# Optimization experiments

Hardware: AMD Instinct MI355X
Metric: run time of the kernel (lower is better)

## Reference

```python
import jax, jax.numpy as jnp
import numpy as np

EMBED_DIM = 1024
NUM_HEADS = 16
HEAD_DIM = EMBED_DIM // NUM_HEADS


def setup_inputs() -> dict:
    key = jax.random.key(0)
    kx, kw1, kb1, kw2, kb2 = jax.random.split(key, 5)
    D = EMBED_DIM
    # torch nn.Linear default init: U(-1/sqrt(in), 1/sqrt(in)); use scaled uniform
    lim = 1.0 / np.sqrt(D)
    return {
        "x": jax.random.normal(kx, (2, 2048, D), dtype=jnp.float32),
        "w_qkv": jax.random.uniform(kw1, (D, 3 * D), jnp.float32, -lim, lim),
        "b_qkv": jax.random.uniform(kb1, (3 * D,), jnp.float32, -lim, lim),
        "w_o": jax.random.uniform(kw2, (D, D), jnp.float32, -lim, lim),
        "b_o": jax.random.uniform(kb2, (D,), jnp.float32, -lim, lim),
    }


def reference(x, w_qkv, b_qkv, w_o, b_o):
    B, S, D = x.shape
    H, hd = NUM_HEADS, HEAD_DIM
    qkv = x @ w_qkv + b_qkv                       # [B,S,3D]
    qkv = qkv.reshape(B, S, H, 3, hd)             # per-head [q|k|v] blocks of size hd
    q = qkv[:, :, :, 0].transpose(0, 2, 1, 3)     # [B,H,S,hd]
    k = qkv[:, :, :, 1].transpose(0, 2, 1, 3)
    v = qkv[:, :, :, 2].transpose(0, 2, 1, 3)
    scale = hd ** -0.5
    scores = jnp.einsum('bhqd,bhkd->bhqk', q, k) * scale
    attn = jax.nn.softmax(scores, axis=-1)
    out = jnp.einsum('bhqk,bhkd->bhqd', attn, v)  # [B,H,S,hd]
    out = out.transpose(0, 2, 1, 3).reshape(B, S, D)
    return out @ w_o + b_o
```

## Files before the change

kernel.cpp:

```cpp
#include <hip/hip_runtime.h>

typedef __attribute__((ext_vector_type(8))) _Float16 half8;
typedef __attribute__((ext_vector_type(4))) _Float16 half4;
typedef __attribute__((ext_vector_type(4))) float f32x4;
typedef __attribute__((ext_vector_type(16))) float f32x16;
typedef __attribute__((ext_vector_type(4))) int i32x4;

typedef __attribute__((address_space(1))) void* gptr_t;
typedef __attribute__((address_space(3))) void* lptr_t;
#define GLL16(g, l) __builtin_amdgcn_global_load_lds((gptr_t)(g), (lptr_t)(l), 16, 0, 0)

__device__ __forceinline__ float fast_exp2(float x) {
  float r;
  asm volatile("v_exp_f32 %0, %1" : "=v"(r) : "v"(x));
  return r;
}


__global__ void prep_kernel(const float* __restrict__ x, _Float16* __restrict__ xh,
                            const float* __restrict__ w_qkv, _Float16* __restrict__ wqkvT,
                            const float* __restrict__ w_o, _Float16* __restrict__ woT) {
  __shared__ _Float16 lds[64][72];
  const int bid = blockIdx.x;
  const int t = threadIdx.x;
  if (bid < 4096) {
    size_t i = (size_t)bid * 256 + t;
    float4 v = *reinterpret_cast<const float4*>(x + i * 4);
    half4 o = { (_Float16)v.x, (_Float16)v.y, (_Float16)v.z, (_Float16)v.w };
    *reinterpret_cast<half4*>(xh + i * 4) = o;
    return;
  }
  const float* w; _Float16* wt; int N, bx, by;
  if (bid < 4096 + 768) { int b = bid - 4096; w = w_qkv; wt = wqkvT; N = 3072; bx = b % 48; by = b / 48; }
  else                  { int b = bid - 4864; w = w_o;   wt = woT;   N = 1024; bx = b & 15; by = b >> 4; }
  const int n0 = bx * 64, k0 = by * 64;
#pragma unroll
  for (int rep = 0; rep < 4; ++rep) {
    int k = rep * 16 + (t >> 4);
    int nc = (t & 15) * 4;
    float4 v = *reinterpret_cast<const float4*>(&w[(size_t)(k0 + k) * N + n0 + nc]);
    lds[nc + 0][k] = (_Float16)v.x;
    lds[nc + 1][k] = (_Float16)v.y;
    lds[nc + 2][k] = (_Float16)v.z;
    lds[nc + 3][k] = (_Float16)v.w;
  }
  __syncthreads();
#pragma unroll
  for (int rep = 0; rep < 2; ++rep) {
    int ch = rep * 256 + t;
    int n = ch >> 3, kc = ch & 7;
    half8 o = *reinterpret_cast<const half8*>(&lds[n][kc * 8]);
    *reinterpret_cast<half8*>(&wt[(size_t)(n0 + n) * 1024 + k0 + kc * 8]) = o;
  }
}


__global__ __launch_bounds__(256, 4)
void gemm_qkv(const _Float16* __restrict__ A, const _Float16* __restrict__ Bt,
              const float* __restrict__ bias,
              _Float16* __restrict__ qh, _Float16* __restrict__ kh,
              _Float16* __restrict__ vT) {
  __shared__ __align__(16) _Float16 Ah[128 * 64];
  __shared__ __align__(16) _Float16 Bh[128 * 64];
  const int t = threadIdx.x;
  const int w = t >> 6, ln = t & 63, G = ln >> 4, c = ln & 15;
  const int lid = blockIdx.y * 24 + blockIdx.x;
  const int swz = (lid & 7) * 96 + (lid >> 3);
  const int bx = swz % 24, by = swz / 24;
  const int m0 = by * 128, n0 = bx * 128;
  const int wr = w >> 1, wc = w & 1;
  f32x4 acc[4][4] = {};
  for (int kt = 0; kt < 1024; kt += 64) {
#pragma unroll
    for (int i = 0; i < 4; ++i) {
      int ch = i * 256 + t;
      int row = ch >> 3, kc = ch & 7;
      int kk = kt + ((kc ^ (row & 7)) << 3);
      int ldsbase = (i * 256 + w * 64) * 8;
      GLL16(A + (size_t)(m0 + row) * 1024 + kk, Ah + ldsbase);
      GLL16(Bt + (size_t)(n0 + row) * 1024 + kk, Bh + ldsbase);
    }
    __syncthreads();
    half8 aF[2][4], bF[2][4];
#pragma unroll
    for (int ks = 0; ks < 2; ++ks)
#pragma unroll
      for (int i = 0; i < 4; ++i) {
        int ra = wr * 64 + i * 16 + c;
        aF[ks][i] = *reinterpret_cast<const half8*>(&Ah[ra * 64 + (((ks * 4 + G) ^ (ra & 7)) << 3)]);
        int rb = wc * 64 + i * 16 + c;
        bF[ks][i] = *reinterpret_cast<const half8*>(&Bh[rb * 64 + (((ks * 4 + G) ^ (rb & 7)) << 3)]);
      }
#pragma unroll
    for (int ks = 0; ks < 2; ++ks)
#pragma unroll
      for (int mi = 0; mi < 4; ++mi)
#pragma unroll
        for (int ni = 0; ni < 4; ++ni)
          acc[mi][ni] = __builtin_amdgcn_mfma_f32_16x16x32_f16(aF[ks][mi], bF[ks][ni], acc[mi][ni], 0, 0, 0);
    __syncthreads();
  }
  const int mbase = m0 + wr * 64, nbase = n0 + wc * 64;
  const int Gp = ((G & 1) << 1) | (G >> 1);
#pragma unroll
  for (int ni = 0; ni < 4; ++ni) {
    int n = nbase + ni * 16 + c;
    float bv = bias[n];
    int h = n / 192;
    int rem = n - h * 192;
    int tt = rem >> 6, d = rem & 63;
#pragma unroll
    for (int mi = 0; mi < 4; ++mi) {
      if (tt == 2) {
        int mb = mbase + mi * 16;
        int bb = mb >> 11, s0 = mb & 2047;
        size_t bh = (size_t)(bb * 16 + h);
        half4 o = { (_Float16)(acc[mi][ni][0] + bv), (_Float16)(acc[mi][ni][1] + bv),
                    (_Float16)(acc[mi][ni][2] + bv), (_Float16)(acc[mi][ni][3] + bv) };
        *reinterpret_cast<half4*>(&vT[(bh * 64 + d) * 2048 + s0 + 4 * Gp]) = o;
      } else {
#pragma unroll
        for (int r = 0; r < 4; ++r) {
          int m = mbase + mi * 16 + 4 * G + r;
          int bb = m >> 11, s = m & 2047;
          float val = acc[mi][ni][r] + bv;
          size_t bh = (size_t)(bb * 16 + h);
          if (tt == 0) qh[(bh * 2048 + s) * 64 + d] = (_Float16)(val * (0.125f * 1.44269504089f));
          else         kh[(bh * 2048 + s) * 64 + d] = (_Float16)val;
        }
      }
    }
  }
}


__global__ __launch_bounds__(256, 4)
void gemm_o(const _Float16* __restrict__ A, const _Float16* __restrict__ Bt,
            const float* __restrict__ bias, float* __restrict__ outf) {
  __shared__ __align__(16) _Float16 Ah[128 * 64];
  __shared__ __align__(16) _Float16 Bh[64 * 64];
  const int t = threadIdx.x;
  const int w = t >> 6, ln = t & 63, G = ln >> 4, c = ln & 15;
  const int lid = blockIdx.y * 16 + blockIdx.x;
  const int swz = (lid & 7) * 64 + (lid >> 3);
  const int bx = swz & 15, by = swz >> 4;
  const int m0 = by * 128, n0 = bx * 64;
  const int wr = w >> 1, wc = w & 1;
  f32x4 acc[4][2] = {};
  for (int kt = 0; kt < 1024; kt += 64) {
#pragma unroll
    for (int i = 0; i < 4; ++i) {
      int ch = i * 256 + t;
      int row = ch >> 3, kc = ch & 7;
      int kk = kt + ((kc ^ (row & 7)) << 3);
      GLL16(A + (size_t)(m0 + row) * 1024 + kk, Ah + (i * 256 + w * 64) * 8);
    }
#pragma unroll
    for (int i = 0; i < 2; ++i) {
      int ch = i * 256 + t;
      int row = ch >> 3, kc = ch & 7;
      int kk = kt + ((kc ^ (row & 7)) << 3);
      GLL16(Bt + (size_t)(n0 + row) * 1024 + kk, Bh + (i * 256 + w * 64) * 8);
    }
    __syncthreads();
    half8 aF[2][4], bF[2][2];
#pragma unroll
    for (int ks = 0; ks < 2; ++ks) {
#pragma unroll
      for (int i = 0; i < 4; ++i) {
        int ra = wr * 64 + i * 16 + c;
        aF[ks][i] = *reinterpret_cast<const half8*>(&Ah[ra * 64 + (((ks * 4 + G) ^ (ra & 7)) << 3)]);
      }
#pragma unroll
      for (int i = 0; i < 2; ++i) {
        int rb = wc * 32 + i * 16 + c;
        bF[ks][i] = *reinterpret_cast<const half8*>(&Bh[rb * 64 + (((ks * 4 + G) ^ (rb & 7)) << 3)]);
      }
    }
#pragma unroll
    for (int ks = 0; ks < 2; ++ks)
#pragma unroll
      for (int mi = 0; mi < 4; ++mi)
#pragma unroll
        for (int ni = 0; ni < 2; ++ni)
          acc[mi][ni] = __builtin_amdgcn_mfma_f32_16x16x32_f16(aF[ks][mi], bF[ks][ni], acc[mi][ni], 0, 0, 0);
    __syncthreads();
  }
  const int mbase = m0 + wr * 64, nbase = n0 + wc * 32;
#pragma unroll
  for (int ni = 0; ni < 2; ++ni) {
    int n = nbase + ni * 16 + c;
    float bv = bias[n];
#pragma unroll
    for (int mi = 0; mi < 4; ++mi)
#pragma unroll
      for (int r = 0; r < 4; ++r) {
        int m = mbase + mi * 16 + 4 * G + r;
        outf[(size_t)m * 1024 + n] = acc[mi][ni][r] + bv;
      }
  }
}


__global__ __launch_bounds__(256, 1)
void attn_kernel(const _Float16* __restrict__ qh, const _Float16* __restrict__ kh,
                 const _Float16* __restrict__ vT, _Float16* __restrict__ ao) {
  __shared__ __align__(16) _Float16 Kt[3][64 * 64];
  __shared__ __align__(16) _Float16 Vt[4][64 * 64];
  const int t = threadIdx.x;
  const int w = t >> 6, ln = t & 63, lo = ln & 31, hi = ln >> 5;
  const int bid = blockIdx.x;
  const int xcd = bid & 7, tt = bid >> 3;
  const int bh = xcd * 4 + (tt >> 4);
  const int qb = tt & 15;
  const int q0 = qb * 128 + w * 32;
  const _Float16* qp = qh + (size_t)bh * 2048 * 64;
  const _Float16* kp = kh + (size_t)bh * 2048 * 64;
  const _Float16* vp = vT + (size_t)bh * 64 * 2048;

  half8 qf[4];
#pragma unroll
  for (int sl = 0; sl < 4; ++sl)
    qf[sl] = *reinterpret_cast<const half8*>(qp + (size_t)(q0 + lo) * 64 + sl * 16 + hi * 8);

  f32x16 O0 = {}, O1 = {};
  f32x16 S0, S1;
  float plsum = 0.f;
  unsigned pk[4][4];

  auto stage = [&](int kb, int vb, int jt) {
#pragma unroll
    for (int i = 0; i < 2; ++i) {
      int ch = i * 256 + t;
      int row = ch >> 3, cc = ch & 7;
      int sw = ((cc ^ ((row ^ (row >> 3)) & 7)) << 3);
      int ldsbase = (i * 256 + w * 64) * 8;
      GLL16(kp + (size_t)(jt + row) * 64 + sw, &Kt[kb][ldsbase]);
      GLL16(vp + (size_t)row * 2048 + jt + sw, &Vt[vb][ldsbase]);
    }
  };

  auto qkt = [&](int kb) {
    f32x16 a = {}, b = {};
#pragma unroll
    for (int sl = 0; sl < 4; ++sl) {
      const int ch = sl * 2 + hi;
      const int r0 = lo, r1 = 32 + lo;
      half8 k0 = *reinterpret_cast<const half8*>(&Kt[kb][r0 * 64 + ((ch ^ ((r0 ^ (r0 >> 3)) & 7)) << 3)]);
      a = __builtin_amdgcn_mfma_f32_32x32x16_f16(k0, qf[sl], a, 0, 0, 0);
      half8 k1 = *reinterpret_cast<const half8*>(&Kt[kb][r1 * 64 + ((ch ^ ((r1 ^ (r1 >> 3)) & 7)) << 3)]);
      b = __builtin_amdgcn_mfma_f32_32x32x16_f16(k1, qf[sl], b, 0, 0, 0);
    }
    S0 = a; S1 = b;
  };

  auto pv = [&](int vb) {
#pragma unroll
    for (int kb2 = 0; kb2 < 4; ++kb2) {
      i32x4 pi = { (int)pk[kb2][0], (int)pk[kb2][1], (int)pk[kb2][2], (int)pk[kb2][3] };
      half8 pf = __builtin_bit_cast(half8, pi);
      const int ch = kb2 * 2 + hi;
      const int r0 = lo, r1 = 32 + lo;
      half8 v0 = *reinterpret_cast<const half8*>(&Vt[vb][r0 * 64 + ((ch ^ ((r0 ^ (r0 >> 3)) & 7)) << 3)]);
      O0 = __builtin_amdgcn_mfma_f32_32x32x16_f16(v0, pf, O0, 0, 0, 0);
      half8 v1 = *reinterpret_cast<const half8*>(&Vt[vb][r1 * 64 + ((ch ^ ((r1 ^ (r1 >> 3)) & 7)) << 3)]);
      O1 = __builtin_amdgcn_mfma_f32_32x32x16_f16(v1, pf, O1, 0, 0, 0);
    }
  };

  auto smpack = [&]() {
    float e0[16], e1[16];
#pragma unroll
    for (int i = 0; i < 16; ++i) e0[i] = fast_exp2(S0[i]);
#pragma unroll
    for (int i = 0; i < 16; ++i) e1[i] = fast_exp2(S1[i]);
    float sm[8];
#pragma unroll
    for (int i = 0; i < 8; ++i) sm[i] = (e0[i] + e0[i + 8]) + (e1[i] + e1[i + 8]);
#pragma unroll
    for (int i = 0; i < 4; ++i) sm[i] += sm[i + 4];
    plsum += (sm[0] + sm[1]) + (sm[2] + sm[3]);
#pragma unroll
    for (int kh2 = 0; kh2 < 2; ++kh2)
#pragma unroll
      for (int j = 0; j < 4; ++j) {
        pk[kh2][j]     = __builtin_bit_cast(unsigned, __builtin_amdgcn_cvt_pkrtz(e0[kh2 * 8 + 2 * j], e0[kh2 * 8 + 2 * j + 1]));
        pk[2 + kh2][j] = __builtin_bit_cast(unsigned, __builtin_amdgcn_cvt_pkrtz(e1[kh2 * 8 + 2 * j], e1[kh2 * 8 + 2 * j + 1]));
      }
  };

  stage(0, 0, 0);
  stage(1, 1, 64);
  stage(2, 2, 128);
  asm volatile("s_waitcnt vmcnt(8)" ::: "memory");
  __builtin_amdgcn_s_barrier();
  qkt(0);
  asm volatile("s_waitcnt vmcnt(4)" ::: "memory");
  __builtin_amdgcn_s_barrier();

  int kb_w = 0, kb_n = 1;
  for (int it = 0; it < 31; ++it) {
    if (it < 29) stage(kb_w, (it + 3) & 3, (it + 3) * 64);
    smpack();
    __builtin_amdgcn_s_setprio(1);
    qkt(kb_n);
    pv(it & 3);
    __builtin_amdgcn_s_setprio(0);
    if (it < 29) asm volatile("s_waitcnt vmcnt(4)" ::: "memory");
    else         asm volatile("s_waitcnt vmcnt(0)" ::: "memory");
    __builtin_amdgcn_s_barrier();
    if (++kb_w == 3) kb_w = 0;
    if (++kb_n == 3) kb_n = 0;
  }
  smpack();
  pv(31 & 3);

  float lsum = plsum + __shfl_xor(plsum, 32);
  float inv = 1.f / lsum;
  const int bb = bh >> 4, hd_i = bh & 15;
  const size_t srow = (size_t)bb * 2048 + q0 + lo;
  _Float16* aob = ao + srow * 1024 + hd_i * 64 + hi * 4;
#pragma unroll
  for (int rq = 0; rq < 4; ++rq) {
    half4 o0 = { (_Float16)(O0[4 * rq] * inv), (_Float16)(O0[4 * rq + 1] * inv),
                 (_Float16)(O0[4 * rq + 2] * inv), (_Float16)(O0[4 * rq + 3] * inv) };
    *reinterpret_cast<half4*>(aob + rq * 8) = o0;
    half4 o1 = { (_Float16)(O1[4 * rq] * inv), (_Float16)(O1[4 * rq + 1] * inv),
                 (_Float16)(O1[4 * rq + 2] * inv), (_Float16)(O1[4 * rq + 3] * inv) };
    *reinterpret_cast<half4*>(aob + 32 + rq * 8) = o1;
  }
}


extern "C" void kernel_launch(void* const* d_in, const int* in_sizes, int n_in,
                              void* d_out, int out_size, void* d_ws, size_t ws_size,
                              hipStream_t stream) {
  const float* x     = (const float*)d_in[0];
  const float* w_qkv = (const float*)d_in[1];
  const float* b_qkv = (const float*)d_in[2];
  const float* w_o   = (const float*)d_in[3];
  const float* b_o   = (const float*)d_in[4];
  float* out = (float*)d_out;
  char* ws = (char*)d_ws;
  _Float16* xh    = (_Float16*)(ws);
  _Float16* wqkvT = (_Float16*)(ws + ((size_t)8  << 20));
  _Float16* woT   = (_Float16*)(ws + ((size_t)14 << 20));
  _Float16* qh    = (_Float16*)(ws + ((size_t)16 << 20));
  _Float16* kh    = (_Float16*)(ws + ((size_t)24 << 20));
  _Float16* vT    = (_Float16*)(ws + ((size_t)32 << 20));
  _Float16* ao    = (_Float16*)(ws + ((size_t)40 << 20));

  prep_kernel<<<5120, 256, 0, stream>>>(x, xh, w_qkv, wqkvT, w_o, woT);
  gemm_qkv<<<dim3(24, 32), 256, 0, stream>>>(xh, wqkvT, b_qkv, qh, kh, vT);
  attn_kernel<<<512, 256, 0, stream>>>(qh, kh, vT, ao);
  gemm_o<<<dim3(16, 32), 256, 0, stream>>>(ao, woT, b_o, out);
}
```

Baseline: 112.2 us.

## Split attention over two key halves and merge partial outputs in a combine kernel

Each (batch, head, query-block) is split into two blocks that each handle half of the keys. The grid doubles to 1024 blocks, and the K and V LDS ring buffers shrink. Each block writes an unnormalized fp16 partial output and its row sums, and a new combine kernel adds the two partials and normalizes them. The goal is more parallelism and occupancy in the attention kernel. The cost is an extra launch, about 24MB of extra global traffic, and a shallower prefetch pipeline that waits on vmcnt(0) every iteration.

Measured after the change: 119.2 us. 1.06x slower.

```diff
diff --git a/kernel.cpp b/kernel.cpp
--- a/kernel.cpp
+++ b/kernel.cpp
@@ -204,19 +204,24 @@
 
 __global__ __launch_bounds__(256, 1)
 void attn_kernel(const _Float16* __restrict__ qh, const _Float16* __restrict__ kh,
-                 const _Float16* __restrict__ vT, _Float16* __restrict__ ao) {
-  __shared__ __align__(16) _Float16 Kt[3][64 * 64];
-  __shared__ __align__(16) _Float16 Vt[4][64 * 64];
+                 const _Float16* __restrict__ vT,
+                 _Float16* __restrict__ On0, _Float16* __restrict__ On1,
+                 float* __restrict__ l0, float* __restrict__ l1) {
+  __shared__ __align__(16) _Float16 Kt[2][64 * 64];
+  __shared__ __align__(16) _Float16 Vt[3][64 * 64];
   const int t = threadIdx.x;
   const int w = t >> 6, ln = t & 63, lo = ln & 31, hi = ln >> 5;
   const int bid = blockIdx.x;
   const int xcd = bid & 7, tt = bid >> 3;
-  const int bh = xcd * 4 + (tt >> 4);
-  const int qb = tt & 15;
+  const int bh = xcd * 4 + (tt >> 5);
+  const int rem = tt & 31;
+  const int qb = rem >> 1, ks = rem & 1;
   const int q0 = qb * 128 + w * 32;
   const _Float16* qp = qh + (size_t)bh * 2048 * 64;
-  const _Float16* kp = kh + (size_t)bh * 2048 * 64;
-  const _Float16* vp = vT + (size_t)bh * 64 * 2048;
+  const _Float16* kp = kh + ((size_t)bh * 2048 + ks * 1024) * 64;
+  const _Float16* vp = vT + (size_t)bh * 64 * 2048 + ks * 1024;
+  _Float16* On = ks ? On1 : On0;
+  float* lb = ks ? l1 : l0;
 
   half8 qf[4];
 #pragma unroll
@@ -291,44 +296,59 @@
 
   stage(0, 0, 0);
   stage(1, 1, 64);
-  stage(2, 2, 128);
-  asm volatile("s_waitcnt vmcnt(8)" ::: "memory");
+  asm volatile("s_waitcnt vmcnt(4)" ::: "memory");
   __builtin_amdgcn_s_barrier();
   qkt(0);
-  asm volatile("s_waitcnt vmcnt(4)" ::: "memory");
+  asm volatile("s_waitcnt vmcnt(0)" ::: "memory");
   __builtin_amdgcn_s_barrier();
 
-  int kb_w = 0, kb_n = 1;
-  for (int it = 0; it < 31; ++it) {
-    if (it < 29) stage(kb_w, (it + 3) & 3, (it + 3) * 64);
+  int vb_r = 0, vb_w = 2;
+  for (int it = 0; it < 15; ++it) {
+    if (it < 14) stage(it & 1, vb_w, (it + 2) * 64);
     smpack();
     __builtin_amdgcn_s_setprio(1);
-    qkt(kb_n);
-    pv(it & 3);
+    qkt((it + 1) & 1);
+    pv(vb_r);
     __builtin_amdgcn_s_setprio(0);
-    if (it < 29) asm volatile("s_waitcnt vmcnt(4)" ::: "memory");
-    else         asm volatile("s_waitcnt vmcnt(0)" ::: "memory");
+    asm volatile("s_waitcnt vmcnt(0)" ::: "memory");
     __builtin_amdgcn_s_barrier();
-    if (++kb_w == 3) kb_w = 0;
-    if (++kb_n == 3) kb_n = 0;
+    if (++vb_r == 3) vb_r = 0;
+    if (++vb_w == 3) vb_w = 0;
   }
   smpack();
-  pv(31 & 3);
+  pv(vb_r);
 
   float lsum = plsum + __shfl_xor(plsum, 32);
-  float inv = 1.f / lsum;
   const int bb = bh >> 4, hd_i = bh & 15;
   const size_t srow = (size_t)bb * 2048 + q0 + lo;
-  _Float16* aob = ao + srow * 1024 + hd_i * 64 + hi * 4;
+  if (hi == 0) lb[(size_t)bh * 2048 + q0 + lo] = lsum;
+  _Float16* aob = On + srow * 1024 + hd_i * 64 + hi * 4;
 #pragma unroll
   for (int rq = 0; rq < 4; ++rq) {
-    half4 o0 = { (_Float16)(O0[4 * rq] * inv), (_Float16)(O0[4 * rq + 1] * inv),
-                 (_Float16)(O0[4 * rq + 2] * inv), (_Float16)(O0[4 * rq + 3] * inv) };
+    half4 o0 = { (_Float16)O0[4 * rq], (_Float16)O0[4 * rq + 1],
+                 (_Float16)O0[4 * rq + 2], (_Float16)O0[4 * rq + 3] };
     *reinterpret_cast<half4*>(aob + rq * 8) = o0;
-    half4 o1 = { (_Float16)(O1[4 * rq] * inv), (_Float16)(O1[4 * rq + 1] * inv),
-                 (_Float16)(O1[4 * rq + 2] * inv), (_Float16)(O1[4 * rq + 3] * inv) };
+    half4 o1 = { (_Float16)O1[4 * rq], (_Float16)O1[4 * rq + 1],
+                 (_Float16)O1[4 * rq + 2], (_Float16)O1[4 * rq + 3] };
     *reinterpret_cast<half4*>(aob + 32 + rq * 8) = o1;
   }
+}
+
+
+__global__ void combine_kernel(const _Float16* __restrict__ On1,
+                               const float* __restrict__ l0, const float* __restrict__ l1,
+                               _Float16* __restrict__ ao ) {
+  size_t idx = ((size_t)blockIdx.x * 256 + threadIdx.x) * 8;
+  int row = (int)(idx >> 10), col = (int)(idx & 1023);
+  int bb = row >> 11, s = row & 2047, h = col >> 6;
+  size_t bq = (size_t)(bb * 16 + h) * 2048 + s;
+  float inv = 1.f / (l0[bq] + l1[bq]);
+  half8 a = *reinterpret_cast<const half8*>(ao + idx);
+  half8 b = *reinterpret_cast<const half8*>(On1 + idx);
+  half8 o;
+#pragma unroll
+  for (int i = 0; i < 8; ++i) o[i] = (_Float16)(((float)a[i] + (float)b[i]) * inv);
+  *reinterpret_cast<half8*>(ao + idx) = o;
 }
 
 
@@ -349,9 +369,13 @@
   _Float16* kh    = (_Float16*)(ws + ((size_t)24 << 20));
   _Float16* vT    = (_Float16*)(ws + ((size_t)32 << 20));
   _Float16* ao    = (_Float16*)(ws + ((size_t)40 << 20));
+  _Float16* On1   = xh;
+  float*    l0    = (float*)(ws + ((size_t)8 << 20));
+  float*    l1    = (float*)(ws + ((size_t)8 << 20) + (256u << 10));
 
   prep_kernel<<<5120, 256, 0, stream>>>(x, xh, w_qkv, wqkvT, w_o, woT);
   gemm_qkv<<<dim3(24, 32), 256, 0, stream>>>(xh, wqkvT, b_qkv, qh, kh, vT);
-  attn_kernel<<<512, 256, 0, stream>>>(qh, kh, vT, ao);
+  attn_kernel<<<1024, 256, 0, stream>>>(qh, kh, vT, ao, On1, l0, l1);
+  combine_kernel<<<2048, 256, 0, stream>>>(On1, l0, l1, ao);
   gemm_o<<<dim3(16, 32), 256, 0, stream>>>(ao, woT, b_o, out);
 }
```

## Load V fragments straight from global into registers instead of staging through LDS

Applied to the files above, without the earlier changes.

Drops the LDS buffer for V in the attention kernel. Each wave now loads its V MFMA fragments directly from global memory into registers, issued after the PV step for the next tile, while only K keeps the LDS ring. The prologue, loop wait counts and tail iterations are reworked to match. This removes LDS writes and reads for V and frees shared memory. In exchange, all four waves read the same V tile separately, which raises L2 traffic, and global load latency can land on the PV critical path.

After: 135.9 us. +21.2%, slower.

```diff
diff --git a/kernel.cpp b/kernel.cpp
--- a/kernel.cpp
+++ b/kernel.cpp
@@ -206,7 +206,6 @@
 void attn_kernel(const _Float16* __restrict__ qh, const _Float16* __restrict__ kh,
                  const _Float16* __restrict__ vT, _Float16* __restrict__ ao) {
   __shared__ __align__(16) _Float16 Kt[3][64 * 64];
-  __shared__ __align__(16) _Float16 Vt[4][64 * 64];
   const int t = threadIdx.x;
   const int w = t >> 6, ln = t & 63, lo = ln & 31, hi = ln >> 5;
   const int bid = blockIdx.x;
@@ -216,7 +215,7 @@
   const int q0 = qb * 128 + w * 32;
   const _Float16* qp = qh + (size_t)bh * 2048 * 64;
   const _Float16* kp = kh + (size_t)bh * 2048 * 64;
-  const _Float16* vp = vT + (size_t)bh * 64 * 2048;
+  const _Float16* vbase = vT + (size_t)bh * 64 * 2048 + (size_t)lo * 2048 + hi * 8;
 
   half8 qf[4];
 #pragma unroll
@@ -225,19 +224,26 @@
 
   f32x16 O0 = {}, O1 = {};
   f32x16 S0, S1;
+  half8 vf[2][4];
   float plsum = 0.f;
   unsigned pk[4][4];
 
-  auto stage = [&](int kb, int vb, int jt) {
+  auto stageK = [&](int kb, int jt) {
 #pragma unroll
     for (int i = 0; i < 2; ++i) {
       int ch = i * 256 + t;
       int row = ch >> 3, cc = ch & 7;
       int sw = ((cc ^ ((row ^ (row >> 3)) & 7)) << 3);
-      int ldsbase = (i * 256 + w * 64) * 8;
-      GLL16(kp + (size_t)(jt + row) * 64 + sw, &Kt[kb][ldsbase]);
-      GLL16(vp + (size_t)row * 2048 + jt + sw, &Vt[vb][ldsbase]);
-    }
+      GLL16(kp + (size_t)(jt + row) * 64 + sw, &Kt[kb][(i * 256 + w * 64) * 8]);
+    }
+  };
+
+  auto loadV = [&](int tile) {
+#pragma unroll
+    for (int dh = 0; dh < 2; ++dh)
+#pragma unroll
+      for (int kb2 = 0; kb2 < 4; ++kb2)
+        vf[dh][kb2] = *reinterpret_cast<const half8*>(vbase + dh * 65536 + tile * 64 + kb2 * 16);
   };
 
   auto qkt = [&](int kb) {
@@ -254,17 +260,13 @@
     S0 = a; S1 = b;
   };
 
-  auto pv = [&](int vb) {
+  auto pv = [&]() {
 #pragma unroll
     for (int kb2 = 0; kb2 < 4; ++kb2) {
       i32x4 pi = { (int)pk[kb2][0], (int)pk[kb2][1], (int)pk[kb2][2], (int)pk[kb2][3] };
       half8 pf = __builtin_bit_cast(half8, pi);
-      const int ch = kb2 * 2 + hi;
-      const int r0 = lo, r1 = 32 + lo;
-      half8 v0 = *reinterpret_cast<const half8*>(&Vt[vb][r0 * 64 + ((ch ^ ((r0 ^ (r0 >> 3)) & 7)) << 3)]);
-      O0 = __builtin_amdgcn_mfma_f32_32x32x16_f16(v0, pf, O0, 0, 0, 0);
-      half8 v1 = *reinterpret_cast<const half8*>(&Vt[vb][r1 * 64 + ((ch ^ ((r1 ^ (r1 >> 3)) & 7)) << 3)]);
-      O1 = __builtin_amdgcn_mfma_f32_32x32x16_f16(v1, pf, O1, 0, 0, 0);
+      O0 = __builtin_amdgcn_mfma_f32_32x32x16_f16(vf[0][kb2], pf, O0, 0, 0, 0);
+      O1 = __builtin_amdgcn_mfma_f32_32x32x16_f16(vf[1][kb2], pf, O1, 0, 0, 0);
     }
   };
 
@@ -289,31 +291,45 @@
       }
   };
 
-  stage(0, 0, 0);
-  stage(1, 1, 64);
-  stage(2, 2, 128);
-  asm volatile("s_waitcnt vmcnt(8)" ::: "memory");
+  loadV(0);
+  stageK(0, 0); stageK(1, 64); stageK(2, 128);
+  asm volatile("s_waitcnt vmcnt(4)" ::: "memory");
   __builtin_amdgcn_s_barrier();
   qkt(0);
-  asm volatile("s_waitcnt vmcnt(4)" ::: "memory");
+  asm volatile("s_waitcnt vmcnt(2)" ::: "memory");
   __builtin_amdgcn_s_barrier();
 
   int kb_w = 0, kb_n = 1;
-  for (int it = 0; it < 31; ++it) {
-    if (it < 29) stage(kb_w, (it + 3) & 3, (it + 3) * 64);
+  for (int it = 0; it < 29; ++it) {
     smpack();
     __builtin_amdgcn_s_setprio(1);
     qkt(kb_n);
-    pv(it & 3);
+    pv();
     __builtin_amdgcn_s_setprio(0);
-    if (it < 29) asm volatile("s_waitcnt vmcnt(4)" ::: "memory");
-    else         asm volatile("s_waitcnt vmcnt(0)" ::: "memory");
+    loadV(it + 1);
+    stageK(kb_w, (it + 3) * 64);
+    asm volatile("s_waitcnt vmcnt(10)" ::: "memory");
     __builtin_amdgcn_s_barrier();
     if (++kb_w == 3) kb_w = 0;
     if (++kb_n == 3) kb_n = 0;
   }
   smpack();
-  pv(31 & 3);
+  __builtin_amdgcn_s_setprio(1);
+  qkt(kb_n);
+  pv();
+  __builtin_amdgcn_s_setprio(0);
+  loadV(30);
+  asm volatile("s_waitcnt vmcnt(8)" ::: "memory");
+  __builtin_amdgcn_s_barrier();
+  if (++kb_n == 3) kb_n = 0;
+  smpack();
+  __builtin_amdgcn_s_setprio(1);
+  qkt(kb_n);
+  pv();
+  __builtin_amdgcn_s_setprio(0);
+  loadV(31);
+  smpack();
+  pv();
 
   float lsum = plsum + __shfl_xor(plsum, 32);
   float inv = 1.f / lsum;
```
